# Optimization experiments

Hardware: AMD Instinct MI355X
Metric: run time of the kernel (lower is better)

Reference implementation:

```python
import jax, jax.numpy as jnp
import numpy as np

N, E, D, R = 100000, 1600000, 64, 16


def setup_inputs() -> dict:
    key = jax.random.key(0)
    k = jax.random.split(key, 8)
    feat = jax.random.normal(k[0], (N, D), dtype=jnp.float32)
    # xavier-uniform-ish scale (gain=sqrt(2), fan_in=fan_out=D) ~ std 0.177
    relation_weight = jax.random.normal(k[1], (R, D, D), dtype=jnp.float32) * 0.17
    relation_embed = jax.random.normal(k[2], (R, D), dtype=jnp.float32)
    W1 = jax.random.normal(k[3], (D, D), dtype=jnp.float32) * 0.1
    W2 = jax.random.normal(k[4], (D, D), dtype=jnp.float32) * 0.1
    src = jax.random.randint(k[5], (E,), 0, N, dtype=jnp.int32)
    dst = jax.random.randint(k[6], (E,), 0, N, dtype=jnp.int32)
    etype = jax.random.randint(k[7], (E,), 0, R, dtype=jnp.int32)
    return {"feat": feat, "relation_weight": relation_weight,
            "relation_embed": relation_embed, "W1": W1, "W2": W2,
            "src": src, "dst": dst, "etype": etype}


def reference(feat, relation_weight, relation_embed, W1, W2, src, dst, etype):
    n = feat.shape[0]
    # Project every node through every relation once ([N,R,D]) instead of
    # materializing the per-edge [E,D,D] weight gather; same math as
    # t_r = h_src @ W_{r(e)}, h_r = h_dst @ W_{r(e)}.
    proj = jnp.einsum('nd,rdo->nro', feat, relation_weight)  # [N,R,D]
    t_r = proj[src, etype]                                   # [E,D]
    h_r = proj[dst, etype]                                   # [E,D]
    # attention logit per edge: <t_r, tanh(h_r + r_embed)>
    att = jnp.sum(t_r * jnp.tanh(h_r + relation_embed[etype]), axis=-1)  # [E]
    # edge softmax over incoming edges of each destination node
    seg_max = jax.ops.segment_max(att, dst, num_segments=n)
    e = jnp.exp(att - seg_max[dst])
    seg_sum = jax.ops.segment_sum(e, dst, num_segments=n)
    a = e / seg_sum[dst]                                     # [E]
    # weighted aggregation of source features
    msgs = feat[src] * a[:, None]                            # [E,D]
    h_nb = jax.ops.segment_sum(msgs, dst, num_segments=n)    # [N,D]
    # Bi-interaction residual (torch leaky_relu default slope 0.01)
    out = (jax.nn.leaky_relu((feat + h_nb) @ W1.T, negative_slope=0.01)
           + jax.nn.leaky_relu((feat * h_nb) @ W2.T, negative_slope=0.01))
    return out
```

## Files before the change

### kernel.cpp

```cpp
#include <hip/hip_runtime.h>
#include <math.h>

#define D 64

typedef __attribute__((ext_vector_type(8))) short bf16x8;
typedef __attribute__((ext_vector_type(4))) float f32x4;

static __device__ __forceinline__ unsigned short f2bf(float f) {
    unsigned int u = __float_as_uint(f);
    unsigned int r = (u + 0x7FFFu + ((u >> 16) & 1u)) >> 16;
    return (unsigned short)r;
}
static __device__ __forceinline__ float bf2f(unsigned short h) {
    return __uint_as_float(((unsigned int)h) << 16);
}

#if defined(__has_builtin)
#if __has_builtin(__builtin_amdgcn_cvt_pk_bf16_f32)
#define HAVE_PK_BF16 1
#endif
#endif

static __device__ __forceinline__ unsigned int pk2bf(float a, float b) {
#ifdef HAVE_PK_BF16
    auto v = __builtin_amdgcn_cvt_pk_bf16_f32(a, b);
    return *(unsigned int*)&v;
#else
    return (unsigned int)f2bf(a) | ((unsigned int)f2bf(b) << 16);
#endif
}

static __device__ __forceinline__ float fast_tanh(float x) {
    float e = __expf(2.f * x);
    float r = __builtin_amdgcn_rcpf(e + 1.f);
    return 1.f - 2.f * r;
}

typedef __attribute__((address_space(1))) const unsigned int as1_uint;
typedef __attribute__((address_space(3))) unsigned int as3_uint;
static __device__ __forceinline__ void dma16(const void* g, void* l) {
    __builtin_amdgcn_global_load_lds((as1_uint*)g, (as3_uint*)l, 16, 0, 0);
}

static __device__ __forceinline__ int exscan_at(const int* __restrict__ tsc,
                                                const int* __restrict__ bofs, int i) {
    return (i == 0) ? 0 : (tsc[i - 1] + bofs[(i - 1) >> 10]);
}

__global__ __launch_bounds__(256) void k_wsplitA(const float* __restrict__ W,
                                                 unsigned short* __restrict__ B1h,
                                                 unsigned short* __restrict__ B1l,
                                                 unsigned short* __restrict__ B2h,
                                                 unsigned short* __restrict__ B2l,
                                                 const float* __restrict__ W1,
                                                 const float* __restrict__ W2,
                                                 unsigned short* __restrict__ F1h,
                                                 unsigned short* __restrict__ F1l,
                                                 unsigned short* __restrict__ F2h,
                                                 unsigned short* __restrict__ F2l,
                                                 int R) {
    int idx = blockIdx.x * 256 + threadIdx.x;
    int per_g = R * 512;
    if (idx < 2 * per_g) {
        int g = idx / per_g;
        int rest = idx % per_g;
        int r = rest >> 9;
        int rest2 = rest & 511;
        int c = rest2 >> 7;
        int kb = (rest2 >> 6) & 1;
        int lane = rest2 & 63;
        int m = lane & 15, q = lane >> 4;
        bf16x8 hv, lv;
        #pragma unroll
        for (int j = 0; j < 8; ++j) {
            float v;
            if (g == 0) v = W[(size_t)r * 4096 + (kb * 32 + q * 8 + j) * 64 + (c * 16 + m)];
            else        v = W[(size_t)r * 4096 + (c * 16 + m) * 64 + (kb * 32 + q * 8 + j)];
            unsigned short h = f2bf(v);
            hv[j] = (short)h;
            lv[j] = (short)f2bf(v - bf2f(h));
        }
        size_t off = ((((size_t)r * 4 + c) * 2 + kb) * 64 + lane) * 8;
        unsigned short* ph = (g == 0) ? B1h : B2h;
        unsigned short* pl = (g == 0) ? B1l : B2l;
        *(bf16x8*)&ph[off] = hv;
        *(bf16x8*)&pl[off] = lv;
    } else {
        int idx2 = idx - 2 * per_g;
        if (idx2 >= 1024) return;
        int g = idx2 >> 9;
        int rest2 = idx2 & 511;
        int c = rest2 >> 7;
        int kb = (rest2 >> 6) & 1;
        int lane = rest2 & 63;
        int m = lane & 15, q = lane >> 4;
        const float* Wx = g ? W2 : W1;
        bf16x8 hv, lv;
        #pragma unroll
        for (int j = 0; j < 8; ++j) {
            float v = Wx[(c * 16 + m) * 64 + kb * 32 + q * 8 + j];
            unsigned short h = f2bf(v);
            hv[j] = (short)h;
            lv[j] = (short)f2bf(v - bf2f(h));
        }
        size_t off = (((size_t)c * 2 + kb) * 64 + lane) * 8;
        unsigned short* ph = g ? F2h : F1h;
        unsigned short* pl = g ? F2l : F1l;
        *(bf16x8*)&ph[off] = hv;
        *(bf16x8*)&pl[off] = lv;
    }
}

__global__ __launch_bounds__(256) void k_fcastp(const float* __restrict__ feat,
                                                unsigned short* __restrict__ fb,
                                                int N) {
    int idx = blockIdx.x * 256 + threadIdx.x;
    if (idx >= N * 16) return;
    int n = idx >> 4, k = idx & 15;
    union { _Float16 h[4]; uint2 u; } cv;
    #pragma unroll
    for (int c = 0; c < 4; ++c)
        cv.h[c] = (_Float16)feat[(size_t)n * D + c * 16 + k];
    *(uint2*)&fb[(size_t)n * D + k * 4] = cv.u;
}

#define NB3 256

__global__ __launch_bounds__(256) void k_bcount(const int* __restrict__ dst,
                                                int* __restrict__ cnt,
                                                int E, int CH, int NBUK) {
    __shared__ int h[1024];
    const int t = threadIdx.x, blk = blockIdx.x;
    for (int b = t; b < NBUK; b += 256) h[b] = 0;
    __syncthreads();
    const int s0 = blk * CH, s1 = min(E, s0 + CH);
    for (int e = s0 + t; e < s1; e += 256)
        atomicAdd(&h[dst[e] >> 7], 1);
    __syncthreads();
    for (int b = t; b < NBUK; b += 256)
        cnt[(b << 8) | blk] = h[b];
}

__global__ __launch_bounds__(256) void k_bscatter(const int* __restrict__ src,
                                                  const int* __restrict__ dst,
                                                  const int* __restrict__ etype,
                                                  const int* __restrict__ tsc,
                                                  const int* __restrict__ bofs,
                                                  int* __restrict__ ebuf,
                                                  int E, int CH, int NBUK) {
    __shared__ int cur[1024];
    const int t = threadIdx.x, blk = blockIdx.x;
    for (int b = t; b < NBUK; b += 256) cur[b] = exscan_at(tsc, bofs, (b << 8) | blk);
    __syncthreads();
    const int s0 = blk * CH, s1 = min(E, s0 + CH);
    for (int e = s0 + t; e < s1; e += 256) {
        int d = dst[e];
        int b = d >> 7;
        int pos = atomicAdd(&cur[b], 1);
        unsigned int pk = (unsigned int)src[e] | ((unsigned int)etype[e] << 20)
                        | ((unsigned int)(d & 127) << 25);
        ebuf[pos] = (int)pk;
    }
}

__global__ __launch_bounds__(256) void k_bcsr(const int* __restrict__ ebuf,
                                              const int* __restrict__ tsc,
                                              const int* __restrict__ bofs,
                                              int* __restrict__ offsets,
                                              int* __restrict__ spack,
                                              int N, int E, int NBUK) {
    __shared__ int sdeg[128], sincl[128], scur[128];
    const int t = threadIdx.x, b = blockIdx.x;
    const int s0 = exscan_at(tsc, bofs, b << 8);
    const int s1 = exscan_at(tsc, bofs, (b + 1) << 8);
    if (t < 128) { sdeg[t] = 0; }
    __syncthreads();
    for (int e = s0 + t; e < s1; e += 256)
        atomicAdd(&sdeg[((unsigned int)ebuf[e]) >> 25], 1);
    __syncthreads();
    if (t < 128) sincl[t] = sdeg[t];
    __syncthreads();
    for (int off = 1; off < 128; off <<= 1) {
        int v = 0;
        if (t < 128 && t >= off) v = sincl[t - off];
        __syncthreads();
        if (t < 128) sincl[t] += v;
        __syncthreads();
    }
    if (t < 128) {
        int excl = sincl[t] - sdeg[t];
        scur[t] = s0 + excl;
        int n = (b << 7) + t;
        if (n < N) offsets[n] = s0 + excl;
    }
    if (b == NBUK - 1 && t == 0) offsets[N] = E;
    __syncthreads();
    for (int e = s0 + t; e < s1; e += 256) {
        unsigned int pk = (unsigned int)ebuf[e];
        int i = pk >> 25;
        int p = atomicAdd(&scur[i], 1);
        spack[p] = (int)(pk & 0x01FFFFFFu);
    }
}

__global__ __launch_bounds__(1024) void k_scan1(const int* __restrict__ deg, int* __restrict__ tscan,
                                                int* __restrict__ bsum, int N) {
    __shared__ int s[1024];
    const int t = threadIdx.x;
    const int i = blockIdx.x * 1024 + t;
    int v = (i < N) ? deg[i] : 0;
    s[t] = v;
    __syncthreads();
    for (int off = 1; off < 1024; off <<= 1) {
        int tmp = (t >= off) ? s[t - off] : 0;
        __syncthreads();
        s[t] += tmp;
        __syncthreads();
    }
    if (i < N) tscan[i] = s[t];
    if (t == 1023) bsum[blockIdx.x] = s[1023];
}

__global__ __launch_bounds__(1024) void k_scan2(const int* __restrict__ bsum, int* __restrict__ bofs, int NB) {
    __shared__ int s[1024];
    const int t = threadIdx.x;
    int carry = 0;
    for (int b0 = 0; b0 < NB; b0 += 1024) {
        int i = b0 + t;
        int v = (i < NB) ? bsum[i] : 0;
        s[t] = v;
        __syncthreads();
        for (int off = 1; off < 1024; off <<= 1) {
            int tmp = (t >= off) ? s[t - off] : 0;
            __syncthreads();
            s[t] += tmp;
            __syncthreads();
        }
        if (i < NB) bofs[i] = carry + s[t] - v;
        int tot = s[1023];
        __syncthreads();
        carry += tot;
    }
}

__global__ __launch_bounds__(256, 4) void k_projv(const float* __restrict__ feat,
                                                  const unsigned short* __restrict__ B1h,
                                                  const unsigned short* __restrict__ B1l,
                                                  const unsigned short* __restrict__ B2h,
                                                  const unsigned short* __restrict__ B2l,
                                                  const float* __restrict__ emb,
                                                  unsigned short* __restrict__ V,
                                                  int N, int R, int nrq) {
    const int tile = blockIdx.x / nrq;
    const int rq   = blockIdx.x % nrq;
    const int rbase = rq * 4;
    const int rcnt  = (R - rbase < 4) ? (R - rbase) : 4;
    const int n0 = tile * 128;
    __shared__ __align__(16) unsigned short Bbuf[32][512];
    __shared__ __align__(16) unsigned short Us[4][1024];
    const int t = threadIdx.x;
    const int lane = t & 63, w = t >> 6;
    const int m = lane & 15, q = lane >> 4;

    bf16x8 ah[2][2], al[2][2];
    #pragma unroll
    for (int s = 0; s < 2; ++s) {
        int n = n0 + w * 32 + s * 16 + m;
        const float* rowp = feat + (size_t)n * D;
        #pragma unroll
        for (int kb = 0; kb < 2; ++kb) {
            int d0 = kb * 32 + q * 8;
            float4 v0 = make_float4(0.f, 0.f, 0.f, 0.f), v1 = v0;
            if (n < N) { v0 = *(const float4*)(rowp + d0); v1 = *(const float4*)(rowp + d0 + 4); }
            float vals[8] = {v0.x, v0.y, v0.z, v0.w, v1.x, v1.y, v1.z, v1.w};
            bf16x8 hv, lv;
            #pragma unroll
            for (int j = 0; j < 8; ++j) {
                unsigned short h = f2bf(vals[j]);
                hv[j] = (short)h;
                lv[j] = (short)f2bf(vals[j] - bf2f(h));
            }
            ah[s][kb] = hv; al[s][kb] = lv;
        }
    }

    auto stage_half = [&](int r, int half) {
        const unsigned short* arr = half ? ((w < 2) ? B2h : B2l)
                                         : ((w < 2) ? B1h : B1l);
        const unsigned short* gp = arr + (size_t)r * 4096 + (size_t)(w & 1) * 2048 + lane * 8;
        unsigned short* lp = &Bbuf[half * 16 + (w >> 1) * 8 + (w & 1) * 4][0];
        #pragma unroll
        for (int i = 0; i < 4; ++i)
            dma16(gp + i * 512, lp + i * 512);
    };

    stage_half(rbase, 0);
    stage_half(rbase, 1);
    __syncthreads();

    for (int rr = 0; rr < rcnt; ++rr) {
        const int r = rbase + rr;
        float em[4];
        #pragma unroll
        for (int c = 0; c < 4; ++c) em[c] = emb[r * 64 + c * 16 + m];

        f32x4 acc[4][2];
        #pragma unroll
        for (int c = 0; c < 4; ++c)
            #pragma unroll
            for (int s = 0; s < 2; ++s) acc[c][s] = (f32x4){0.f, 0.f, 0.f, 0.f};
        #pragma unroll
        for (int c = 0; c < 4; ++c) {
            bf16x8 bh[2], bl[2];
            #pragma unroll
            for (int kb = 0; kb < 2; ++kb) {
                bh[kb] = *(const bf16x8*)&Bbuf[c * 2 + kb][lane * 8];
                bl[kb] = *(const bf16x8*)&Bbuf[8 + c * 2 + kb][lane * 8];
            }
            #pragma unroll
            for (int s = 0; s < 2; ++s)
                #pragma unroll
                for (int kb = 0; kb < 2; ++kb) {
                    acc[c][s] = __builtin_amdgcn_mfma_f32_16x16x32_bf16(ah[s][kb], bh[kb], acc[c][s], 0, 0, 0);
                    acc[c][s] = __builtin_amdgcn_mfma_f32_16x16x32_bf16(al[s][kb], bh[kb], acc[c][s], 0, 0, 0);
                    acc[c][s] = __builtin_amdgcn_mfma_f32_16x16x32_bf16(ah[s][kb], bl[kb], acc[c][s], 0, 0, 0);
                }
        }

        __syncthreads();
        if (rr + 1 < rcnt) stage_half(r + 1, 0);

        #pragma unroll
        for (int s = 0; s < 2; ++s) {
            #pragma unroll
            for (int c = 0; c < 4; ++c) {
                int o = c * 16 + m;
                int kb2 = o >> 5;
                int q2 = (o >> 3) & 3;
                int j = o & 7;
                int Fb = kb2 * 64 + q2 * 16 + q * 4;
                #pragma unroll
                for (int i = 0; i < 4; i += 2) {
                    float t0 = fast_tanh(acc[c][s][i] + em[c]);
                    float t1 = fast_tanh(acc[c][s][i + 1] + em[c]);
                    unsigned int pk = pk2bf(t0, t1);
                    Us[w][((Fb + i) ^ q2) * 8 + j]     = (unsigned short)(pk & 0xFFFF);
                    Us[w][((Fb + i + 1) ^ q2) * 8 + j] = (unsigned short)(pk >> 16);
                }
            }

            bf16x8 ua[2];
            #pragma unroll
            for (int kb = 0; kb < 2; ++kb) {
                int F = kb * 64 + lane;
                ua[kb] = *(const bf16x8*)&Us[w][(F ^ (lane >> 4)) * 8];
            }
            f32x4 acc2[4];
            #pragma unroll
            for (int c = 0; c < 4; ++c) acc2[c] = (f32x4){0.f, 0.f, 0.f, 0.f};
            #pragma unroll
            for (int c = 0; c < 4; ++c) {
                bf16x8 bh[2], bl[2];
                #pragma unroll
                for (int kb = 0; kb < 2; ++kb) {
                    bh[kb] = *(const bf16x8*)&Bbuf[16 + c * 2 + kb][lane * 8];
                    bl[kb] = *(const bf16x8*)&Bbuf[24 + c * 2 + kb][lane * 8];
                }
                #pragma unroll
                for (int kb = 0; kb < 2; ++kb) {
                    acc2[c] = __builtin_amdgcn_mfma_f32_16x16x32_bf16(ua[kb], bh[kb], acc2[c], 0, 0, 0);
                    acc2[c] = __builtin_amdgcn_mfma_f32_16x16x32_bf16(ua[kb], bl[kb], acc2[c], 0, 0, 0);
                }
            }

            #pragma unroll
            for (int i = 0; i < 4; ++i) {
                int n = n0 + w * 32 + s * 16 + q * 4 + i;
                if (n < N) {
                    uint2 pv;
                    pv.x = pk2bf(acc2[0][i], acc2[1][i]);
                    pv.y = pk2bf(acc2[2][i], acc2[3][i]);
                    *(uint2*)&V[((size_t)n * R + r) * 64 + m * 4] = pv;
                }
            }
        }

        __syncthreads();
        if (rr + 1 < rcnt) stage_half(r + 1, 1);
    }
}

__global__ __launch_bounds__(256) void k_fused2(const unsigned short* __restrict__ V,
                                                const unsigned short* __restrict__ fb,
                                                const int* __restrict__ offsets,
                                                const int* __restrict__ spack,
                                                float* __restrict__ h_nb,
                                                int N, int R) {
    const int lane = threadIdx.x & 63;
    const int wav  = threadIdx.x >> 6;
    const int g    = lane >> 4;
    const int k    = lane & 15;
    const int n = blockIdx.x * 4 + wav;
    __shared__ __align__(16) unsigned short vlds[4][1024];

    if (n < N) {
        const unsigned short* gp = V + (size_t)n * 1024 + lane * 8;
        dma16(gp,       &vlds[wav][0]);
        dma16(gp + 512, &vlds[wav][512]);
    }
    __syncthreads();
    if (n >= N) return;

    const int beg = offsets[n], end = offsets[n + 1];
    float m = -INFINITY, l = 0.f;
    float4 acc = make_float4(0.f, 0.f, 0.f, 0.f);

    for (int cbeg = beg; cbeg < end; cbeg += 16) {
        float pv0, pv1, pv2, pv3;
        uint2 gv0, gv1, gv2, gv3;
        #pragma unroll
        for (int it = 0; it < 4; ++it) {
            int e = cbeg + it * 4 + g;
            bool ok = e < end;
            int pk = spack[ok ? e : end - 1];
            uint2 fvu = *(const uint2*)&fb[(size_t)(pk & 0xFFFFF) * D + k * 4];
            int et = pk >> 20;
            uint2 vvu = *(const uint2*)&vlds[wav][et * 64 + k * 4];
            union { uint2 u; _Float16 h[4]; } cf; cf.u = fvu;
            float d = (float)cf.h[0] * bf2f((unsigned short)(vvu.x & 0xFFFF))
                    + (float)cf.h[1] * bf2f((unsigned short)(vvu.x >> 16))
                    + (float)cf.h[2] * bf2f((unsigned short)(vvu.y & 0xFFFF))
                    + (float)cf.h[3] * bf2f((unsigned short)(vvu.y >> 16));
            d += __shfl_xor(d, 1, 64);
            d += __shfl_xor(d, 2, 64);
            d += __shfl_xor(d, 4, 64);
            d += __shfl_xor(d, 8, 64);
            d = ok ? d : -INFINITY;
            if (it == 0) { pv0 = d; gv0 = fvu; }
            else if (it == 1) { pv1 = d; gv1 = fvu; }
            else if (it == 2) { pv2 = d; gv2 = fvu; }
            else { pv3 = d; gv3 = fvu; }
        }
        float cm = fmaxf(fmaxf(pv0, pv1), fmaxf(pv2, pv3));
        cm = fmaxf(cm, __shfl_xor(cm, 16, 64));
        cm = fmaxf(cm, __shfl_xor(cm, 32, 64));
        float nm = fmaxf(m, cm);
        float scale = __expf(m - nm);
        float w0 = __expf(pv0 - nm);
        float w1 = __expf(pv1 - nm);
        float w2 = __expf(pv2 - nm);
        float w3 = __expf(pv3 - nm);
        float cs = w0 + w1 + w2 + w3;
        cs += __shfl_xor(cs, 16, 64);
        cs += __shfl_xor(cs, 32, 64);
        l = l * scale + cs;
        acc.x *= scale; acc.y *= scale; acc.z *= scale; acc.w *= scale;
        {
            union { uint2 u; _Float16 h[4]; } c0, c1, c2, c3;
            c0.u = gv0; c1.u = gv1; c2.u = gv2; c3.u = gv3;
            acc.x += w0 * (float)c0.h[0] + w1 * (float)c1.h[0]
                   + w2 * (float)c2.h[0] + w3 * (float)c3.h[0];
            acc.y += w0 * (float)c0.h[1] + w1 * (float)c1.h[1]
                   + w2 * (float)c2.h[1] + w3 * (float)c3.h[1];
            acc.z += w0 * (float)c0.h[2] + w1 * (float)c1.h[2]
                   + w2 * (float)c2.h[2] + w3 * (float)c3.h[2];
            acc.w += w0 * (float)c0.h[3] + w1 * (float)c1.h[3]
                   + w2 * (float)c2.h[3] + w3 * (float)c3.h[3];
        }
        m = nm;
    }

    acc.x += __shfl_xor(acc.x, 16, 64);
    acc.y += __shfl_xor(acc.y, 16, 64);
    acc.z += __shfl_xor(acc.z, 16, 64);
    acc.w += __shfl_xor(acc.w, 16, 64);
    acc.x += __shfl_xor(acc.x, 32, 64);
    acc.y += __shfl_xor(acc.y, 32, 64);
    acc.z += __shfl_xor(acc.z, 32, 64);
    acc.w += __shfl_xor(acc.w, 32, 64);
    float inv = (l != 0.f) ? 1.f / l : 0.f;
    if (lane < 16) {
        h_nb[(size_t)n * D + 0 * 16 + k] = acc.x * inv;
        h_nb[(size_t)n * D + 1 * 16 + k] = acc.y * inv;
        h_nb[(size_t)n * D + 2 * 16 + k] = acc.z * inv;
        h_nb[(size_t)n * D + 3 * 16 + k] = acc.w * inv;
    }
}

__global__ __launch_bounds__(256, 2) void k_final(const float* __restrict__ feat,
                                                  const float* __restrict__ h_nb,
                                                  const unsigned short* __restrict__ F1h,
                                                  const unsigned short* __restrict__ F1l,
                                                  const unsigned short* __restrict__ F2h,
                                                  const unsigned short* __restrict__ F2l,
                                                  float* __restrict__ out, int N) {
    const int n0 = blockIdx.x * 128;
    __shared__ __align__(16) unsigned short Wlds[4][4096];
    const int t = threadIdx.x;
    const int lane = t & 63, w = t >> 6;
    const int m = lane & 15, q = lane >> 4;

    const unsigned short* warr = (w == 0) ? F1h : (w == 1) ? F1l : (w == 2) ? F2h : F2l;
    #pragma unroll
    for (int i = 0; i < 8; ++i)
        dma16(warr + i * 512 + lane * 8, &Wlds[w][i * 512]);

    bf16x8 sh[2][2], sl[2][2], ph[2][2], pl[2][2];
    #pragma unroll
    for (int s = 0; s < 2; ++s) {
        int n = n0 + w * 32 + s * 16 + m;
        const float* fp = feat + (size_t)n * D;
        const float* hp = h_nb + (size_t)n * D;
        #pragma unroll
        for (int kb = 0; kb < 2; ++kb) {
            int d0 = kb * 32 + q * 8;
            float4 f0 = make_float4(0.f, 0.f, 0.f, 0.f), f1 = f0, h0 = f0, h1 = f0;
            if (n < N) {
                f0 = *(const float4*)(fp + d0); f1 = *(const float4*)(fp + d0 + 4);
                h0 = *(const float4*)(hp + d0); h1 = *(const float4*)(hp + d0 + 4);
            }
            float fv[8] = {f0.x, f0.y, f0.z, f0.w, f1.x, f1.y, f1.z, f1.w};
            float hv[8] = {h0.x, h0.y, h0.z, h0.w, h1.x, h1.y, h1.z, h1.w};
            bf16x8 a, b, c2, d2;
            #pragma unroll
            for (int j = 0; j < 8; ++j) {
                float xs = fv[j] + hv[j];
                float xp = fv[j] * hv[j];
                unsigned short hs = f2bf(xs);
                unsigned short hp2 = f2bf(xp);
                a[j]  = (short)hs;
                b[j]  = (short)f2bf(xs - bf2f(hs));
                c2[j] = (short)hp2;
                d2[j] = (short)f2bf(xp - bf2f(hp2));
            }
            sh[s][kb] = a; sl[s][kb] = b; ph[s][kb] = c2; pl[s][kb] = d2;
        }
    }
    __syncthreads();

    f32x4 a1[4][2], a2[4][2];
    #pragma unroll
    for (int c = 0; c < 4; ++c)
        #pragma unroll
        for (int s = 0; s < 2; ++s) {
            a1[c][s] = (f32x4){0.f, 0.f, 0.f, 0.f};
            a2[c][s] = (f32x4){0.f, 0.f, 0.f, 0.f};
        }
    #pragma unroll
    for (int c = 0; c < 4; ++c) {
        bf16x8 b1h[2], b1l[2], b2h[2], b2l[2];
        #pragma unroll
        for (int kb = 0; kb < 2; ++kb) {
            int o = (c * 2 + kb) * 512 + lane * 8;
            b1h[kb] = *(const bf16x8*)&Wlds[0][o];
            b1l[kb] = *(const bf16x8*)&Wlds[1][o];
            b2h[kb] = *(const bf16x8*)&Wlds[2][o];
            b2l[kb] = *(const bf16x8*)&Wlds[3][o];
        }
        #pragma unroll
        for (int kb = 0; kb < 2; ++kb)
            #pragma unroll
            for (int s = 0; s < 2; ++s) {
                a1[c][s] = __builtin_amdgcn_mfma_f32_16x16x32_bf16(sh[s][kb], b1h[kb], a1[c][s], 0, 0, 0);
                a1[c][s] = __builtin_amdgcn_mfma_f32_16x16x32_bf16(sl[s][kb], b1h[kb], a1[c][s], 0, 0, 0);
                a1[c][s] = __builtin_amdgcn_mfma_f32_16x16x32_bf16(sh[s][kb], b1l[kb], a1[c][s], 0, 0, 0);
                a2[c][s] = __builtin_amdgcn_mfma_f32_16x16x32_bf16(ph[s][kb], b2h[kb], a2[c][s], 0, 0, 0);
                a2[c][s] = __builtin_amdgcn_mfma_f32_16x16x32_bf16(pl[s][kb], b2h[kb], a2[c][s], 0, 0, 0);
                a2[c][s] = __builtin_amdgcn_mfma_f32_16x16x32_bf16(ph[s][kb], b2l[kb], a2[c][s], 0, 0, 0);
            }
    }

    #pragma unroll
    for (int s = 0; s < 2; ++s)
        #pragma unroll
        for (int i = 0; i < 4; ++i) {
            int n = n0 + w * 32 + s * 16 + q * 4 + i;
            if (n < N) {
                #pragma unroll
                for (int c = 0; c < 4; ++c) {
                    float o1 = a1[c][s][i];
                    float o2 = a2[c][s][i];
                    o1 = (o1 > 0.f) ? o1 : 0.01f * o1;
                    o2 = (o2 > 0.f) ? o2 : 0.01f * o2;
                    out[(size_t)n * D + c * 16 + m] = o1 + o2;
                }
            }
        }
}

extern "C" void kernel_launch(void* const* d_in, const int* in_sizes, int n_in,
                              void* d_out, int out_size, void* d_ws, size_t ws_size,
                              hipStream_t stream) {
    const float* feat  = (const float*)d_in[0];
    const float* relW  = (const float*)d_in[1];
    const float* relE  = (const float*)d_in[2];
    const float* W1    = (const float*)d_in[3];
    const float* W2    = (const float*)d_in[4];
    const int*   src   = (const int*)d_in[5];
    const int*   dst   = (const int*)d_in[6];
    const int*   etype = (const int*)d_in[7];
    float* out = (float*)d_out;

    const int N = in_sizes[0] / D;
    const int R = in_sizes[2] / D;
    const int E = in_sizes[5];

    char* w = (char*)d_ws;
    size_t off = 0;
    auto alloc = [&](size_t bytes) -> void* {
        void* p = w + off;
        off = (off + bytes + 255) & ~(size_t)255;
        return p;
    };
    unsigned short* varr = (unsigned short*)alloc((size_t)N * R * D * sizeof(unsigned short));
    float* h_nb   = (float*)alloc((size_t)N * D * sizeof(float));
    int* offsets  = (int*)alloc((size_t)(N + 1) * sizeof(int));
    int* bsum     = (int*)alloc(2048 * sizeof(int));
    int* bofs     = (int*)alloc(2048 * sizeof(int));
    int* spack    = (int*)alloc((size_t)E * sizeof(int));
    unsigned short* fb = (unsigned short*)alloc((size_t)N * D * sizeof(unsigned short));
    size_t wfrag = (size_t)R * 4 * 2 * 64 * 8;
    unsigned short* B1h = (unsigned short*)alloc(wfrag * sizeof(unsigned short));
    unsigned short* B1l = (unsigned short*)alloc(wfrag * sizeof(unsigned short));
    unsigned short* B2h = (unsigned short*)alloc(wfrag * sizeof(unsigned short));
    unsigned short* B2l = (unsigned short*)alloc(wfrag * sizeof(unsigned short));
    unsigned short* F1h = (unsigned short*)alloc(4096 * sizeof(unsigned short));
    unsigned short* F1l = (unsigned short*)alloc(4096 * sizeof(unsigned short));
    unsigned short* F2h = (unsigned short*)alloc(4096 * sizeof(unsigned short));
    unsigned short* F2l = (unsigned short*)alloc(4096 * sizeof(unsigned short));
    (void)ws_size; (void)n_in; (void)out_size;

    const int NBUK = (N + 127) >> 7;
    const int CH   = (E + NB3 - 1) / NB3;
    const int L    = NBUK << 8;
    int* ebuf = (int*)varr;
    int* cnt  = ebuf + E;
    int* tsc  = cnt + L;
    const int NBscan = (L + 1023) / 1024;

    const int nrq = (R + 3) / 4;
    const int ntiles = (N + 127) / 128;
    const int nW = 2 * R * 512 + 1024;

    k_wsplitA<<<(nW + 255) / 256, 256, 0, stream>>>(relW, B1h, B1l, B2h, B2l,
                                                    W1, W2, F1h, F1l, F2h, F2l, R);
    k_fcastp<<<(N * 16 + 255) / 256, 256, 0, stream>>>(feat, fb, N);
    k_bcount<<<NB3, 256, 0, stream>>>(dst, cnt, E, CH, NBUK);
    k_scan1<<<NBscan, 1024, 0, stream>>>(cnt, tsc, bsum, L);
    k_scan2<<<1, 1024, 0, stream>>>(bsum, bofs, NBscan);
    k_bscatter<<<NB3, 256, 0, stream>>>(src, dst, etype, tsc, bofs, ebuf, E, CH, NBUK);
    k_bcsr<<<NBUK, 256, 0, stream>>>(ebuf, tsc, bofs, offsets, spack, N, E, NBUK);
    k_projv<<<ntiles * nrq, 256, 0, stream>>>(feat, B1h, B1l, B2h, B2l, relE, varr, N, R, nrq);
    k_fused2<<<(N + 3) / 4, 256, 0, stream>>>(varr, fb, offsets, spack, h_nb, N, R);
    k_final<<<(N + 127) / 128, 256, 0, stream>>>(feat, h_nb, F1h, F1l, F2h, F2l, out, N);
}
```

Measured before the change: 345.7 us.

## Precompute bf16 hi/lo feature split in merged prep kernel, split projv launch

Merges the weight-split and fp16 feature-cast kernels into a single prep kernel. That kernel also precomputes the bf16 hi/lo split of feat into scratch space borrowed from h_nb, so k_projv loads prepared fragments instead of converting fp32 features in every relation-quad block. The projection launch is split into two half-grid launches. The aim is to drop one launch and avoid redundant per-block conversion, at the cost of extra writes and reads of two N×D bf16 arrays and one more launch.

```diff
diff --git a/kernel.cpp b/kernel.cpp
--- a/kernel.cpp
+++ b/kernel.cpp
@@ -47,19 +47,52 @@
     return (i == 0) ? 0 : (tsc[i - 1] + bofs[(i - 1) >> 10]);
 }
 
-__global__ __launch_bounds__(256) void k_wsplitA(const float* __restrict__ W,
-                                                 unsigned short* __restrict__ B1h,
-                                                 unsigned short* __restrict__ B1l,
-                                                 unsigned short* __restrict__ B2h,
-                                                 unsigned short* __restrict__ B2l,
-                                                 const float* __restrict__ W1,
-                                                 const float* __restrict__ W2,
-                                                 unsigned short* __restrict__ F1h,
-                                                 unsigned short* __restrict__ F1l,
-                                                 unsigned short* __restrict__ F2h,
-                                                 unsigned short* __restrict__ F2l,
-                                                 int R) {
+__global__ __launch_bounds__(256) void k_prep(const float* __restrict__ W,
+                                              unsigned short* __restrict__ B1h,
+                                              unsigned short* __restrict__ B1l,
+                                              unsigned short* __restrict__ B2h,
+                                              unsigned short* __restrict__ B2l,
+                                              const float* __restrict__ W1,
+                                              const float* __restrict__ W2,
+                                              unsigned short* __restrict__ F1h,
+                                              unsigned short* __restrict__ F1l,
+                                              unsigned short* __restrict__ F2h,
+                                              unsigned short* __restrict__ F2l,
+                                              const float* __restrict__ feat,
+                                              unsigned short* __restrict__ fb,
+                                              unsigned short* __restrict__ fh,
+                                              unsigned short* __restrict__ fl,
+                                              int R, int N) {
     int idx = blockIdx.x * 256 + threadIdx.x;
+    const int nb = N * 16;
+    const int nc = N * 8;
+    if (idx < nb) {
+        int n = idx >> 4, k = idx & 15;
+        union { _Float16 h[4]; uint2 u; } cv;
+        #pragma unroll
+        for (int c = 0; c < 4; ++c)
+            cv.h[c] = (_Float16)feat[(size_t)n * D + c * 16 + k];
+        *(uint2*)&fb[(size_t)n * D + k * 4] = cv.u;
+        return;
+    }
+    idx -= nb;
+    if (idx < nc) {
+        int n = idx >> 3, ch = idx & 7;
+        const float* p = feat + (size_t)n * D + ch * 8;
+        float4 v0 = *(const float4*)p, v1 = *(const float4*)(p + 4);
+        float vals[8] = {v0.x, v0.y, v0.z, v0.w, v1.x, v1.y, v1.z, v1.w};
+        bf16x8 hv, lv;
+        #pragma unroll
+        for (int j = 0; j < 8; ++j) {
+            unsigned short h = f2bf(vals[j]);
+            hv[j] = (short)h;
+            lv[j] = (short)f2bf(vals[j] - bf2f(h));
+        }
+        *(bf16x8*)&fh[(size_t)n * D + ch * 8] = hv;
+        *(bf16x8*)&fl[(size_t)n * D + ch * 8] = lv;
+        return;
+    }
+    idx -= nc;
     int per_g = R * 512;
     if (idx < 2 * per_g) {
         int g = idx / per_g;
@@ -111,19 +144,6 @@
     }
 }
 
-__global__ __launch_bounds__(256) void k_fcastp(const float* __restrict__ feat,
-                                                unsigned short* __restrict__ fb,
-                                                int N) {
-    int idx = blockIdx.x * 256 + threadIdx.x;
-    if (idx >= N * 16) return;
-    int n = idx >> 4, k = idx & 15;
-    union { _Float16 h[4]; uint2 u; } cv;
-    #pragma unroll
-    for (int c = 0; c < 4; ++c)
-        cv.h[c] = (_Float16)feat[(size_t)n * D + c * 16 + k];
-    *(uint2*)&fb[(size_t)n * D + k * 4] = cv.u;
-}
-
 #define NB3 256
 
 __global__ __launch_bounds__(256) void k_bcount(const int* __restrict__ dst,
@@ -243,15 +263,16 @@
     }
 }
 
-__global__ __launch_bounds__(256, 4) void k_projv(const float* __restrict__ feat,
+__global__ __launch_bounds__(256, 4) void k_projv(const unsigned short* __restrict__ fh,
+                                                  const unsigned short* __restrict__ fl,
                                                   const unsigned short* __restrict__ B1h,
                                                   const unsigned short* __restrict__ B1l,
                                                   const unsigned short* __restrict__ B2h,
                                                   const unsigned short* __restrict__ B2l,
                                                   const float* __restrict__ emb,
                                                   unsigned short* __restrict__ V,
-                                                  int N, int R, int nrq) {
-    const int tile = blockIdx.x / nrq;
+                                                  int N, int R, int nrq, int tile0) {
+    const int tile = tile0 + blockIdx.x / nrq;
     const int rq   = blockIdx.x % nrq;
     const int rbase = rq * 4;
     const int rcnt  = (R - rbase < 4) ? (R - rbase) : 4;
@@ -266,21 +287,17 @@
     #pragma unroll
     for (int s = 0; s < 2; ++s) {
         int n = n0 + w * 32 + s * 16 + m;
-        const float* rowp = feat + (size_t)n * D;
+        bool ok = n < N;
         #pragma unroll
         for (int kb = 0; kb < 2; ++kb) {
             int d0 = kb * 32 + q * 8;
-            float4 v0 = make_float4(0.f, 0.f, 0.f, 0.f), v1 = v0;
-            if (n < N) { v0 = *(const float4*)(rowp + d0); v1 = *(const float4*)(rowp + d0 + 4); }
-            float vals[8] = {v0.x, v0.y, v0.z, v0.w, v1.x, v1.y, v1.z, v1.w};
-            bf16x8 hv, lv;
-            #pragma unroll
-            for (int j = 0; j < 8; ++j) {
-                unsigned short h = f2bf(vals[j]);
-                hv[j] = (short)h;
-                lv[j] = (short)f2bf(vals[j] - bf2f(h));
-            }
-            ah[s][kb] = hv; al[s][kb] = lv;
+            if (ok) {
+                ah[s][kb] = *(const bf16x8*)&fh[(size_t)n * D + d0];
+                al[s][kb] = *(const bf16x8*)&fl[(size_t)n * D + d0];
+            } else {
+                #pragma unroll
+                for (int j = 0; j < 8; ++j) { ah[s][kb][j] = 0; al[s][kb][j] = 0; }
+            }
         }
     }
 
@@ -630,6 +647,9 @@
     unsigned short* F2l = (unsigned short*)alloc(4096 * sizeof(unsigned short));
     (void)ws_size; (void)n_in; (void)out_size;
 
+    unsigned short* fh = (unsigned short*)h_nb;
+    unsigned short* fl = fh + (size_t)N * D;
+
     const int NBUK = (N + 127) >> 7;
     const int CH   = (E + NB3 - 1) / NB3;
     const int L    = NBUK << 8;
@@ -640,17 +660,19 @@
 
     const int nrq = (R + 3) / 4;
     const int ntiles = (N + 127) / 128;
-    const int nW = 2 * R * 512 + 1024;
-
-    k_wsplitA<<<(nW + 255) / 256, 256, 0, stream>>>(relW, B1h, B1l, B2h, B2l,
-                                                    W1, W2, F1h, F1l, F2h, F2l, R);
-    k_fcastp<<<(N * 16 + 255) / 256, 256, 0, stream>>>(feat, fb, N);
+    const int half1 = ntiles / 2;
+    const int nPrep = N * 16 + N * 8 + 2 * R * 512 + 1024;
+
+    k_prep<<<(nPrep + 255) / 256, 256, 0, stream>>>(relW, B1h, B1l, B2h, B2l,
+                                                    W1, W2, F1h, F1l, F2h, F2l,
+                                                    feat, fb, fh, fl, R, N);
     k_bcount<<<NB3, 256, 0, stream>>>(dst, cnt, E, CH, NBUK);
     k_scan1<<<NBscan, 1024, 0, stream>>>(cnt, tsc, bsum, L);
     k_scan2<<<1, 1024, 0, stream>>>(bsum, bofs, NBscan);
     k_bscatter<<<NB3, 256, 0, stream>>>(src, dst, etype, tsc, bofs, ebuf, E, CH, NBUK);
     k_bcsr<<<NBUK, 256, 0, stream>>>(ebuf, tsc, bofs, offsets, spack, N, E, NBUK);
-    k_projv<<<ntiles * nrq, 256, 0, stream>>>(feat, B1h, B1l, B2h, B2l, relE, varr, N, R, nrq);
+    k_projv<<<half1 * nrq, 256, 0, stream>>>(fh, fl, B1h, B1l, B2h, B2l, relE, varr, N, R, nrq, 0);
+    k_projv<<<(ntiles - half1) * nrq, 256, 0, stream>>>(fh, fl, B1h, B1l, B2h, B2l, relE, varr, N, R, nrq, half1);
     k_fused2<<<(N + 3) / 4, 256, 0, stream>>>(varr, fb, offsets, spack, h_nb, N, R);
     k_final<<<(N + 127) / 128, 256, 0, stream>>>(feat, h_nb, F1h, F1l, F2h, F2l, out, N);
 }
```

Result: slower. 356.2 us (+3.0%).
